# Optimization experiments

Hardware: AMD Instinct MI355X
Metric: run time of the kernel (lower is better)

The kernel has to match this reference:

```python
import jax, jax.numpy as jnp
import numpy as np

B, IN_DIM, T, H = 16384, 4096, 6, 256
ALPHA = 0.1


def _prune_l1(w, amount=0.5):
    # emulate torch.nn.utils.prune.l1_unstructured: zero the smallest-|w| fraction
    thr = jnp.quantile(jnp.abs(w).reshape(w.shape[0], -1), amount, axis=1)
    thr = thr.reshape((w.shape[0],) + (1,) * (w.ndim - 1))
    return jnp.where(jnp.abs(w) >= thr, w, 0.0)


def setup_inputs() -> dict:
    key = jax.random.key(0)
    ks = jax.random.split(key, 12)
    s1 = 1.0 / np.sqrt(IN_DIM)
    s2 = 1.0 / np.sqrt(H)
    headW1 = jax.random.uniform(ks[0], (T, H, IN_DIM), minval=-s1, maxval=s1)
    headW1 = _prune_l1(headW1, 0.5)  # prune applied to first Linear of each head
    headb1 = jax.random.uniform(ks[1], (T, H), minval=-s1, maxval=s1)
    headW2 = jax.random.uniform(ks[2], (T, H, H), minval=-s2, maxval=s2)
    headb2 = jax.random.uniform(ks[3], (T, H), minval=-s2, maxval=s2)
    task_queries = jax.random.normal(ks[4], (T, H))
    keyW = jax.random.uniform(ks[5], (H, H), minval=-s2, maxval=s2)
    keyb = jax.random.uniform(ks[6], (H,), minval=-s2, maxval=s2)
    valW = jax.random.uniform(ks[7], (H, H), minval=-s2, maxval=s2)
    valb = jax.random.uniform(ks[8], (H,), minval=-s2, maxval=s2)
    bias = jnp.asarray(2.0, dtype=jnp.float32)
    x = jax.random.normal(ks[9], (B, IN_DIM), dtype=jnp.float32)
    return {"x": x, "headW1": headW1, "headb1": headb1, "headW2": headW2,
            "headb2": headb2, "task_queries": task_queries, "keyW": keyW,
            "keyb": keyb, "valW": valW, "valb": valb, "bias": bias}


def reference(x, headW1, headb1, headW2, headb2, task_queries, keyW, keyb, valW, valb, bias):
    # per-task heads (all heads see the full feature set): [B,T,H]
    h = jax.nn.relu(jnp.einsum("bi,thi->bth", x, headW1) + headb1)
    h = jax.nn.relu(jnp.einsum("bth,toh->bto", h, headW2) + headb2)
    K = jnp.einsum("bth,oh->bto", h, keyW) + keyb  # [B,T,H]
    V = jnp.einsum("bth,oh->bto", h, valW) + valb  # [B,T,H]
    logits = jnp.einsum("qh,bkh->bqk", task_queries, K) / jnp.sqrt(jnp.float32(H))
    m = logits.max(axis=2, keepdims=True) + 1e-8
    W_s = jax.nn.softmax(jnp.eye(T, dtype=logits.dtype) + ALPHA * (logits / m), axis=2)
    attended = jnp.einsum("bqk,bkh->bqh", W_s, V)  # [B,T,H]
    y1_logits = attended.mean(axis=-1)  # [B,T]
    y1_probs = jax.nn.sigmoid(y1_logits - bias)
    return jnp.clip(y1_probs, 1e-7, 1.0 - 1e-7)
```

## Files before the change

### kernel.cpp

```cpp
#include <hip/hip_runtime.h>
#include <hip/hip_bf16.h>


typedef float    f32x4 __attribute__((ext_vector_type(4)));
typedef short    s16x8 __attribute__((ext_vector_type(8)));
typedef unsigned short u16x4 __attribute__((ext_vector_type(4)));

__global__ void M3H_64587718197825_kernel() {}

__device__ __forceinline__ unsigned short bf16rn(float x) {
    unsigned u = __float_as_uint(x);
    return (unsigned short)((u + 0x7FFFu + ((u >> 16) & 1u)) >> 16);
}
__device__ __forceinline__ float bf16tof(unsigned short h) {
    return __uint_as_float(((unsigned)h) << 16);
}


__device__ __forceinline__ void stage_lds16(const unsigned short* src, int ld,
                                            unsigned short* lds, int tid)
{
#pragma unroll
    for (int t = 0; t < 2; ++t) {
        int c  = t * 256 + tid;
        int r  = c >> 2;
        int cr = c & 3;
        int s  = (r + (r >> 2)) & 3;
        long long g = (long long)r * ld + ((cr ^ s) << 3);
        __builtin_amdgcn_global_load_lds(
            (const __attribute__((address_space(1))) unsigned int*)(const void*)(src + g),
            (__attribute__((address_space(3))) unsigned int*)(void*)(lds + (c << 3)),
            16, 0, 0);
    }
}

__device__ __forceinline__ void stage_split_a(const float* Atile, int lda,
                                              unsigned short* sAh, unsigned short* sAl,
                                              int tid)
{
    int r = tid >> 1;
    int h = tid & 1;
    const float* ap = Atile + (long long)r * lda + (h << 4);
    float4 v0 = *(const float4*)(ap + 0);
    float4 v1 = *(const float4*)(ap + 4);
    float4 v2 = *(const float4*)(ap + 8);
    float4 v3 = *(const float4*)(ap + 12);
    float xs[16];
    xs[0]=v0.x; xs[1]=v0.y; xs[2]=v0.z;  xs[3]=v0.w;
    xs[4]=v1.x; xs[5]=v1.y; xs[6]=v1.z;  xs[7]=v1.w;
    xs[8]=v2.x; xs[9]=v2.y; xs[10]=v2.z; xs[11]=v2.w;
    xs[12]=v3.x; xs[13]=v3.y; xs[14]=v3.z; xs[15]=v3.w;
    s16x8 hv0, hv1, lv0, lv1;
#pragma unroll
    for (int i = 0; i < 8; ++i) {
        unsigned short hb = bf16rn(xs[i]);
        hv0[i] = (short)hb;
        lv0[i] = (short)bf16rn(xs[i] - bf16tof(hb));
    }
#pragma unroll
    for (int i = 0; i < 8; ++i) {
        unsigned short hb = bf16rn(xs[8 + i]);
        hv1[i] = (short)hb;
        lv1[i] = (short)bf16rn(xs[8 + i] - bf16tof(hb));
    }
    int s  = (r + (r >> 2)) & 3;
    int c0 = ((h << 1) | 0) ^ s;
    int c1 = ((h << 1) | 1) ^ s;
    int base = r << 5;
    *(s16x8*)(sAh + base + (c0 << 3)) = hv0;
    *(s16x8*)(sAh + base + (c1 << 3)) = hv1;
    *(s16x8*)(sAl + base + (c0 << 3)) = lv0;
    *(s16x8*)(sAl + base + (c1 << 3)) = lv1;
}

template<bool SPLIT_A, bool WRITE_SPLIT>
__global__ __launch_bounds__(256, 4) void gemm_bf16x3(
    const float* A32, const unsigned short* Ah, const unsigned short* Al,
    const unsigned short* Bh, const unsigned short* Bl,
    const float* bias, float* C32, unsigned short* Ch, unsigned short* Cl,
    int K, int lda, int ldb, int ldc,
    long long aOffZ, long long bOffZ, long long cOffZ, long long biasOffZ)
{
    int z = blockIdx.z;
    if constexpr (SPLIT_A) {
        A32 += (long long)z * aOffZ;
    } else {
        Ah += (long long)z * aOffZ;
        Al += (long long)z * aOffZ;
    }
    Bh += (long long)z * bOffZ;
    Bl += (long long)z * bOffZ;
    bias += (long long)z * biasOffZ;
    if constexpr (WRITE_SPLIT) {
        Ch += (long long)z * cOffZ;
        Cl += (long long)z * cOffZ;
    } else {
        C32 += (long long)z * cOffZ;
    }

    __shared__ __attribute__((aligned(16))) unsigned short sAh[4096];
    __shared__ __attribute__((aligned(16))) unsigned short sAl[4096];
    __shared__ __attribute__((aligned(16))) unsigned short sBh[4096];
    __shared__ __attribute__((aligned(16))) unsigned short sBl[4096];

    int nwg = gridDim.x * gridDim.y;
    int lin = blockIdx.y * gridDim.x + blockIdx.x;
    int qq = nwg >> 3, rr = nwg & 7;
    int xcd = lin & 7, idx = lin >> 3;
    int swz = (xcd < rr ? xcd * (qq + 1) : rr * (qq + 1) + (xcd - rr) * qq) + idx;
    const int tm = (swz / gridDim.x) * 128;
    const int tn = (swz % gridDim.x) * 128;

    const int tid  = threadIdx.x;
    const int lane = tid & 63;
    const int wid  = tid >> 6;
    const int wm = (wid & 1) << 6;
    const int wn = (wid >> 1) << 6;
    const int fr = lane & 15;
    const int fk = lane >> 4;
    const int swz8 = ((fk ^ ((fr + (fr >> 2)) & 3)) << 3);

    f32x4 acc[4][4];
    const f32x4 zero = {0.f, 0.f, 0.f, 0.f};
#pragma unroll
    for (int i = 0; i < 4; ++i)
#pragma unroll
        for (int j = 0; j < 4; ++j)
            acc[i][j] = zero;

    for (int k0 = 0; k0 < K; k0 += 32) {
        if constexpr (SPLIT_A) {
            stage_split_a(A32 + (long long)tm * lda + k0, lda, sAh, sAl, tid);
        } else {
            stage_lds16(Ah + (long long)tm * lda + k0, lda, sAh, tid);
            stage_lds16(Al + (long long)tm * lda + k0, lda, sAl, tid);
        }
        stage_lds16(Bh + (long long)tn * ldb + k0, ldb, sBh, tid);
        stage_lds16(Bl + (long long)tn * ldb + k0, ldb, sBl, tid);
        __syncthreads();

        s16x8 bh[4], bl[4];
#pragma unroll
        for (int ni = 0; ni < 4; ++ni) {
            int off = (wn + ni * 16 + fr) * 32 + swz8;
            bh[ni] = *(const s16x8*)(sBh + off);
            bl[ni] = *(const s16x8*)(sBl + off);
        }
#pragma unroll
        for (int mi = 0; mi < 4; ++mi) {
            int off = (wm + mi * 16 + fr) * 32 + swz8;
            s16x8 ah = *(const s16x8*)(sAh + off);
            s16x8 al = *(const s16x8*)(sAl + off);
#pragma unroll
            for (int ni = 0; ni < 4; ++ni) {
                acc[mi][ni] = __builtin_amdgcn_mfma_f32_16x16x32_bf16(ah, bh[ni], acc[mi][ni], 0, 0, 0);
                acc[mi][ni] = __builtin_amdgcn_mfma_f32_16x16x32_bf16(ah, bl[ni], acc[mi][ni], 0, 0, 0);
                acc[mi][ni] = __builtin_amdgcn_mfma_f32_16x16x32_bf16(al, bh[ni], acc[mi][ni], 0, 0, 0);
            }
        }
        __syncthreads();
    }

#pragma unroll
    for (int mi = 0; mi < 4; ++mi) {
        int crow = tm + wm + mi * 16 + fk * 4;
#pragma unroll
        for (int ni = 0; ni < 4; ++ni) {
            int ccol = tn + wn + ni * 16 + fr;
            float bv = bias[ccol];
#pragma unroll
            for (int rr2 = 0; rr2 < 4; ++rr2) {
                float v = acc[mi][ni][rr2] + bv;
                v = v > 0.f ? v : 0.f;
                long long ci = (long long)(crow + rr2) * ldc + ccol;
                if constexpr (WRITE_SPLIT) {
                    unsigned short hb = bf16rn(v);
                    Ch[ci] = hb;
                    Cl[ci] = bf16rn(v - bf16tof(hb));
                } else {
                    C32[ci] = v;
                }
            }
        }
    }
}

__global__ void split_ws(const float* in, unsigned short* hi, unsigned short* lo, int n4)
{
    for (int i = blockIdx.x * 256 + threadIdx.x; i < n4; i += gridDim.x * 256) {
        float4 v = ((const float4*)in)[i];
        float xs[4] = {v.x, v.y, v.z, v.w};
        u16x4 hv, lv;
#pragma unroll
        for (int j = 0; j < 4; ++j) {
            unsigned short hb = bf16rn(xs[j]);
            hv[j] = hb;
            lv[j] = bf16rn(xs[j] - bf16tof(hb));
        }
        ((u16x4*)hi)[i] = hv;
        ((u16x4*)lo)[i] = lv;
    }
}

__global__ void precompute(const float* tq, const float* keyW, const float* keyb,
                           const float* valW, const float* valb,
                           float* qk, float* qb, float* vbar, float* vbbar)
{
    __shared__ float tqs[1536];
    int h = threadIdx.x;
    for (int i = h; i < 1536; i += 256) tqs[i] = tq[i];
    __syncthreads();
    float acc0 = 0.f, acc1 = 0.f, acc2 = 0.f, acc3 = 0.f, acc4 = 0.f, acc5 = 0.f;
    float vb = 0.f;
    for (int o = 0; o < 256; ++o) {
        float kw = keyW[o * 256 + h];
        float vw = valW[o * 256 + h];
        acc0 += tqs[0 * 256 + o] * kw;
        acc1 += tqs[1 * 256 + o] * kw;
        acc2 += tqs[2 * 256 + o] * kw;
        acc3 += tqs[3 * 256 + o] * kw;
        acc4 += tqs[4 * 256 + o] * kw;
        acc5 += tqs[5 * 256 + o] * kw;
        vb += vw;
    }
    qk[0 * 256 + h] = acc0;
    qk[1 * 256 + h] = acc1;
    qk[2 * 256 + h] = acc2;
    qk[3 * 256 + h] = acc3;
    qk[4 * 256 + h] = acc4;
    qk[5 * 256 + h] = acc5;
    vbar[h] = vb * (1.0f / 256.0f);
    if (h < 6) {
        float s = 0.f;
        for (int o = 0; o < 256; ++o) s += tq[h * 256 + o] * keyb[o];
        qb[h] = s;
    }
    if (h == 6) {
        float s = 0.f;
        for (int o = 0; o < 256; ++o) s += valb[o];
        vbbar[0] = s * (1.0f / 256.0f);
    }
}

__global__ void dots(const float* h2, const float* qk, const float* qb,
                     const float* vbar, const float* vbbar,
                     float* L, float* Vm)
{
    __shared__ float U[7][256];
    __shared__ float qbs[8];
    int tid = threadIdx.x;
    for (int i = tid; i < 1792; i += 256)
        U[i >> 8][i & 255] = (i < 1536) ? qk[i] : vbar[i & 255];
    if (tid < 6) qbs[tid] = qb[tid];
    if (tid == 6) qbs[6] = vbbar[0];
    __syncthreads();
    int row = blockIdx.x * 256 + tid;
    const float* hr = h2 + (long long)row * 256;
    float a0 = 0.f, a1 = 0.f, a2 = 0.f, a3 = 0.f, a4 = 0.f, a5 = 0.f, a6 = 0.f;
    for (int i = 0; i < 256; i += 4) {
        float4 v = *(const float4*)(hr + i);
        float xs[4];
        xs[0] = v.x; xs[1] = v.y; xs[2] = v.z; xs[3] = v.w;
        for (int j = 0; j < 4; ++j) {
            float x = xs[j];
            int c = i + j;
            a0 += x * U[0][c];
            a1 += x * U[1][c];
            a2 += x * U[2][c];
            a3 += x * U[3][c];
            a4 += x * U[4][c];
            a5 += x * U[5][c];
            a6 += x * U[6][c];
        }
    }
    int b = row / 6, k = row - b * 6;
    float* Lr = L + (long long)b * 36 + k;
    Lr[0 * 6]  = (a0 + qbs[0]) * 0.0625f;
    Lr[1 * 6]  = (a1 + qbs[1]) * 0.0625f;
    Lr[2 * 6]  = (a2 + qbs[2]) * 0.0625f;
    Lr[3 * 6]  = (a3 + qbs[3]) * 0.0625f;
    Lr[4 * 6]  = (a4 + qbs[4]) * 0.0625f;
    Lr[5 * 6]  = (a5 + qbs[5]) * 0.0625f;
    Vm[row] = a6 + qbs[6];
}

__global__ void attn(const float* L, const float* Vm, const float* biasp, float* out)
{
    int b = blockIdx.x * 256 + threadIdx.x;
    float bias = biasp[0];
    float l[36], vm[6];
    const float* Lr = L + (long long)b * 36;
    for (int i = 0; i < 36; ++i) l[i] = Lr[i];
    for (int k = 0; k < 6; ++k) vm[k] = Vm[(long long)b * 6 + k];
    for (int q = 0; q < 6; ++q) {
        float m = l[q * 6];
        for (int k = 1; k < 6; ++k) m = fmaxf(m, l[q * 6 + k]);
        m += 1e-8f;
        float arg[6];
        float mx = -3.402823e38f;
        for (int k = 0; k < 6; ++k) {
            arg[k] = (k == q ? 1.0f : 0.0f) + 0.1f * l[q * 6 + k] / m;
            mx = fmaxf(mx, arg[k]);
        }
        float s = 0.f, y = 0.f;
        for (int k = 0; k < 6; ++k) {
            float e = expf(arg[k] - mx);
            s += e;
            y += e * vm[k];
        }
        y /= s;
        float p = 1.0f / (1.0f + expf(-(y - bias)));
        p = fminf(fmaxf(p, 1e-7f), 1.0f - 1e-7f);
        out[(long long)b * 6 + q] = p;
    }
}

extern "C" void kernel_launch(void* const* d_in, const int* in_sizes, int n_in,
                              void* d_out, int out_size, void* d_ws, size_t ws_size,
                              hipStream_t stream)
{
    const float* x      = (const float*)d_in[0];
    const float* headW1 = (const float*)d_in[1];
    const float* headb1 = (const float*)d_in[2];
    const float* headW2 = (const float*)d_in[3];
    const float* headb2 = (const float*)d_in[4];
    const float* tq     = (const float*)d_in[5];
    const float* keyW   = (const float*)d_in[6];
    const float* keyb   = (const float*)d_in[7];
    const float* valW   = (const float*)d_in[8];
    const float* valb   = (const float*)d_in[9];
    const float* biasp  = (const float*)d_in[10];
    float* out = (float*)d_out;

    char* w = (char*)d_ws;
    float* qk    = (float*)(w + 0);
    float* vbar  = (float*)(w + 6144);
    float* qb    = (float*)(w + 7168);
    float* vbbar = (float*)(w + 7200);
    unsigned short* h1h = (unsigned short*)(w + 8192);
    unsigned short* h1l = (unsigned short*)(w + 50339840LL);
    float* h2 = (float*)(w + 100671488LL);
    float* L  = (float*)(w + 201334784LL);
    float* Vm = (float*)(w + 203694080LL);
    unsigned short* w1h = (unsigned short*)(w + 204087296LL);
    unsigned short* w1l = (unsigned short*)(w + 216670208LL);
    unsigned short* w2h = (unsigned short*)(w + 229253120LL);
    unsigned short* w2l = (unsigned short*)(w + 230039552LL);

    split_ws<<<1024, 256, 0, stream>>>(headW1, w1h, w1l, 1572864);
    split_ws<<<384,  256, 0, stream>>>(headW2, w2h, w2l, 98304);

    precompute<<<1, 256, 0, stream>>>(tq, keyW, keyb, valW, valb, qk, qb, vbar, vbbar);

    gemm_bf16x3<true, true><<<dim3(12, 128, 1), 256, 0, stream>>>(
        x, nullptr, nullptr, w1h, w1l, headb1, nullptr, h1h, h1l,
        4096, 4096, 4096, 1536, 0, 0, 0, 0);

    gemm_bf16x3<false, false><<<dim3(2, 128, 6), 256, 0, stream>>>(
        nullptr, h1h, h1l, w2h, w2l, headb2, h2, nullptr, nullptr,
        256, 1536, 256, 1536, 256, 65536, 256, 256);

    dots<<<384, 256, 0, stream>>>(h2, qk, qb, vbar, vbbar, L, Vm);
    attn<<<64, 256, 0, stream>>>(L, Vm, biasp, out);
}
```

Before: 1.113 ms.

## Double-buffer LDS tiles to overlap next-tile loads with MFMA compute

Converts the GEMM main loop to a two-stage ping-pong LDS pipeline. The next K-tile's global-to-LDS loads (and the fp32 A loads, held in registers and split into bf16 after compute) are issued before the MFMA work on the current tile, and one barrier per iteration is removed. The aim is to hide global memory latency behind compute. In exchange, LDS use doubles to 64KB and launch bounds drop to 2 blocks per CU, which lowers occupancy and raises register pressure.

```diff
diff --git a/kernel.cpp b/kernel.cpp
--- a/kernel.cpp
+++ b/kernel.cpp
@@ -34,22 +34,32 @@
     }
 }
 
-__device__ __forceinline__ void stage_split_a(const float* Atile, int lda,
-                                              unsigned short* sAh, unsigned short* sAl,
-                                              int tid)
+struct AReg { float4 v0, v1, v2, v3; };
+
+__device__ __forceinline__ AReg stage_a_load(const float* Atile, int lda, int tid)
 {
     int r = tid >> 1;
     int h = tid & 1;
     const float* ap = Atile + (long long)r * lda + (h << 4);
-    float4 v0 = *(const float4*)(ap + 0);
-    float4 v1 = *(const float4*)(ap + 4);
-    float4 v2 = *(const float4*)(ap + 8);
-    float4 v3 = *(const float4*)(ap + 12);
+    AReg a;
+    a.v0 = *(const float4*)(ap + 0);
+    a.v1 = *(const float4*)(ap + 4);
+    a.v2 = *(const float4*)(ap + 8);
+    a.v3 = *(const float4*)(ap + 12);
+    return a;
+}
+
+__device__ __forceinline__ void stage_a_write(const AReg& a,
+                                              unsigned short* sAh, unsigned short* sAl,
+                                              int tid)
+{
+    int r = tid >> 1;
+    int h = tid & 1;
     float xs[16];
-    xs[0]=v0.x; xs[1]=v0.y; xs[2]=v0.z;  xs[3]=v0.w;
-    xs[4]=v1.x; xs[5]=v1.y; xs[6]=v1.z;  xs[7]=v1.w;
-    xs[8]=v2.x; xs[9]=v2.y; xs[10]=v2.z; xs[11]=v2.w;
-    xs[12]=v3.x; xs[13]=v3.y; xs[14]=v3.z; xs[15]=v3.w;
+    xs[0]=a.v0.x; xs[1]=a.v0.y; xs[2]=a.v0.z;  xs[3]=a.v0.w;
+    xs[4]=a.v1.x; xs[5]=a.v1.y; xs[6]=a.v1.z;  xs[7]=a.v1.w;
+    xs[8]=a.v2.x; xs[9]=a.v2.y; xs[10]=a.v2.z; xs[11]=a.v2.w;
+    xs[12]=a.v3.x; xs[13]=a.v3.y; xs[14]=a.v3.z; xs[15]=a.v3.w;
     s16x8 hv0, hv1, lv0, lv1;
 #pragma unroll
     for (int i = 0; i < 8; ++i) {
@@ -74,7 +84,7 @@
 }
 
 template<bool SPLIT_A, bool WRITE_SPLIT>
-__global__ __launch_bounds__(256, 4) void gemm_bf16x3(
+__global__ __launch_bounds__(256, 2) void gemm_bf16x3(
     const float* A32, const unsigned short* Ah, const unsigned short* Al,
     const unsigned short* Bh, const unsigned short* Bl,
     const float* bias, float* C32, unsigned short* Ch, unsigned short* Cl,
@@ -98,10 +108,10 @@
         C32 += (long long)z * cOffZ;
     }
 
-    __shared__ __attribute__((aligned(16))) unsigned short sAh[4096];
-    __shared__ __attribute__((aligned(16))) unsigned short sAl[4096];
-    __shared__ __attribute__((aligned(16))) unsigned short sBh[4096];
-    __shared__ __attribute__((aligned(16))) unsigned short sBl[4096];
+    __shared__ __attribute__((aligned(16))) unsigned short sAh[2][4096];
+    __shared__ __attribute__((aligned(16))) unsigned short sAl[2][4096];
+    __shared__ __attribute__((aligned(16))) unsigned short sBh[2][4096];
+    __shared__ __attribute__((aligned(16))) unsigned short sBl[2][4096];
 
     int nwg = gridDim.x * gridDim.y;
     int lin = blockIdx.y * gridDim.x + blockIdx.x;
@@ -120,6 +130,12 @@
     const int fk = lane >> 4;
     const int swz8 = ((fk ^ ((fr + (fr >> 2)) & 3)) << 3);
 
+    const float* aBase = SPLIT_A ? (A32 + (long long)tm * lda) : nullptr;
+    const unsigned short* ahBase = SPLIT_A ? nullptr : (Ah + (long long)tm * lda);
+    const unsigned short* alBase = SPLIT_A ? nullptr : (Al + (long long)tm * lda);
+    const unsigned short* bhBase = Bh + (long long)tn * ldb;
+    const unsigned short* blBase = Bl + (long long)tn * ldb;
+
     f32x4 acc[4][4];
     const f32x4 zero = {0.f, 0.f, 0.f, 0.f};
 #pragma unroll
@@ -128,35 +144,57 @@
         for (int j = 0; j < 4; ++j)
             acc[i][j] = zero;
 
-    for (int k0 = 0; k0 < K; k0 += 32) {
-        if constexpr (SPLIT_A) {
-            stage_split_a(A32 + (long long)tm * lda + k0, lda, sAh, sAl, tid);
-        } else {
-            stage_lds16(Ah + (long long)tm * lda + k0, lda, sAh, tid);
-            stage_lds16(Al + (long long)tm * lda + k0, lda, sAl, tid);
-        }
-        stage_lds16(Bh + (long long)tn * ldb + k0, ldb, sBh, tid);
-        stage_lds16(Bl + (long long)tn * ldb + k0, ldb, sBl, tid);
-        __syncthreads();
+    if constexpr (SPLIT_A) {
+        AReg a0 = stage_a_load(aBase, lda, tid);
+        stage_a_write(a0, sAh[0], sAl[0], tid);
+    } else {
+        stage_lds16(ahBase, lda, sAh[0], tid);
+        stage_lds16(alBase, lda, sAl[0], tid);
+    }
+    stage_lds16(bhBase, ldb, sBh[0], tid);
+    stage_lds16(blBase, ldb, sBl[0], tid);
+    __syncthreads();
+
+    const int nt = K >> 5;
+    for (int t = 0; t < nt; ++t) {
+        const int P = t & 1, Q = P ^ 1;
+        const bool pf = (t + 1 < nt);
+        const int k1 = (t + 1) << 5;
+
+        AReg nxt;
+        if (pf) {
+            if constexpr (SPLIT_A) {
+                nxt = stage_a_load(aBase + k1, lda, tid);
+            } else {
+                stage_lds16(ahBase + k1, lda, sAh[Q], tid);
+                stage_lds16(alBase + k1, lda, sAl[Q], tid);
+            }
+            stage_lds16(bhBase + k1, ldb, sBh[Q], tid);
+            stage_lds16(blBase + k1, ldb, sBl[Q], tid);
+        }
 
         s16x8 bh[4], bl[4];
 #pragma unroll
         for (int ni = 0; ni < 4; ++ni) {
             int off = (wn + ni * 16 + fr) * 32 + swz8;
-            bh[ni] = *(const s16x8*)(sBh + off);
-            bl[ni] = *(const s16x8*)(sBl + off);
+            bh[ni] = *(const s16x8*)(sBh[P] + off);
+            bl[ni] = *(const s16x8*)(sBl[P] + off);
         }
 #pragma unroll
         for (int mi = 0; mi < 4; ++mi) {
             int off = (wm + mi * 16 + fr) * 32 + swz8;
-            s16x8 ah = *(const s16x8*)(sAh + off);
-            s16x8 al = *(const s16x8*)(sAl + off);
+            s16x8 ah = *(const s16x8*)(sAh[P] + off);
+            s16x8 al = *(const s16x8*)(sAl[P] + off);
 #pragma unroll
             for (int ni = 0; ni < 4; ++ni) {
                 acc[mi][ni] = __builtin_amdgcn_mfma_f32_16x16x32_bf16(ah, bh[ni], acc[mi][ni], 0, 0, 0);
                 acc[mi][ni] = __builtin_amdgcn_mfma_f32_16x16x32_bf16(ah, bl[ni], acc[mi][ni], 0, 0, 0);
                 acc[mi][ni] = __builtin_amdgcn_mfma_f32_16x16x32_bf16(al, bh[ni], acc[mi][ni], 0, 0, 0);
             }
+        }
+
+        if constexpr (SPLIT_A) {
+            if (pf) stage_a_write(nxt, sAh[Q], sAl[Q], tid);
         }
         __syncthreads();
     }
```

Result: slower. 1.219 ms (+9.6%).

## Fuse key/value projection dots into second GEMM epilogue with atomic accumulation

Applied to the files above, without the earlier changes.

The second GEMM's epilogue now applies bias and ReLU, projects each output row onto the six query-key vectors and the mean value vector, reduces across lanes with shuffles, and atomically adds into L and Vm. This removes the fp32 h2 round trip through memory and the separate dots kernel. A zeroing kernel for L/Vm is added, precompute is spread over 7 blocks, and launch bounds drop from 4 to 2 waves per SIMD, which may lower occupancy in the first GEMM. Atomic float adds make the summation order nondeterministic.

```diff
diff --git a/kernel.cpp b/kernel.cpp
--- a/kernel.cpp
+++ b/kernel.cpp
@@ -73,11 +73,13 @@
     *(s16x8*)(sAl + base + (c1 << 3)) = lv1;
 }
 
-template<bool SPLIT_A, bool WRITE_SPLIT>
-__global__ __launch_bounds__(256, 4) void gemm_bf16x3(
+template<bool SPLIT_A, bool WRITE_SPLIT, bool FUSE>
+__global__ __launch_bounds__(256, 2) void gemm_bf16x3(
     const float* A32, const unsigned short* Ah, const unsigned short* Al,
     const unsigned short* Bh, const unsigned short* Bl,
     const float* bias, float* C32, unsigned short* Ch, unsigned short* Cl,
+    const float* qk, const float* qb, const float* vbar, const float* vbbar,
+    float* L, float* Vm,
     int K, int lda, int ldb, int ldc,
     long long aOffZ, long long bOffZ, long long cOffZ, long long biasOffZ)
 {
@@ -94,7 +96,7 @@
     if constexpr (WRITE_SPLIT) {
         Ch += (long long)z * cOffZ;
         Cl += (long long)z * cOffZ;
-    } else {
+    } else if constexpr (!FUSE) {
         C32 += (long long)z * cOffZ;
     }
 
@@ -161,24 +163,72 @@
         __syncthreads();
     }
 
-#pragma unroll
-    for (int mi = 0; mi < 4; ++mi) {
-        int crow = tm + wm + mi * 16 + fk * 4;
+    if constexpr (FUSE) {
+        float Ur[4][7];
+        float biasv[4];
 #pragma unroll
         for (int ni = 0; ni < 4; ++ni) {
             int ccol = tn + wn + ni * 16 + fr;
-            float bv = bias[ccol];
-#pragma unroll
-            for (int rr2 = 0; rr2 < 4; ++rr2) {
-                float v = acc[mi][ni][rr2] + bv;
+            biasv[ni] = bias[ccol];
+#pragma unroll
+            for (int j = 0; j < 6; ++j) Ur[ni][j] = qk[j * 256 + ccol];
+            Ur[ni][6] = vbar[ccol];
+        }
+        float qbl = 0.f;
+        if (fr < 6) qbl = qb[fr];
+        else if (fr == 6) qbl = vbbar[0];
+        const bool addc = ((tn + wn) == 0);
+#pragma unroll
+        for (int r = 0; r < 16; ++r) {
+            const int mi = r >> 2, rr2 = r & 3;
+            int brow = tm + wm + mi * 16 + fk * 4 + rr2;
+            float p[7] = {0.f, 0.f, 0.f, 0.f, 0.f, 0.f, 0.f};
+#pragma unroll
+            for (int ni = 0; ni < 4; ++ni) {
+                float v = acc[mi][ni][rr2] + biasv[ni];
                 v = v > 0.f ? v : 0.f;
-                long long ci = (long long)(crow + rr2) * ldc + ccol;
-                if constexpr (WRITE_SPLIT) {
-                    unsigned short hb = bf16rn(v);
-                    Ch[ci] = hb;
-                    Cl[ci] = bf16rn(v - bf16tof(hb));
-                } else {
-                    C32[ci] = v;
+#pragma unroll
+                for (int j = 0; j < 7; ++j) p[j] += v * Ur[ni][j];
+            }
+#pragma unroll
+            for (int m = 1; m < 16; m <<= 1)
+#pragma unroll
+                for (int j = 0; j < 7; ++j) p[j] += __shfl_xor(p[j], m, 64);
+            float mine = p[0];
+            mine = (fr == 1) ? p[1] : mine;
+            mine = (fr == 2) ? p[2] : mine;
+            mine = (fr == 3) ? p[3] : mine;
+            mine = (fr == 4) ? p[4] : mine;
+            mine = (fr == 5) ? p[5] : mine;
+            mine = (fr == 6) ? p[6] : mine;
+            if (fr < 6) {
+                float val = (mine + (addc ? qbl : 0.f)) * 0.0625f;
+                atomicAdd(&L[(long long)brow * 36 + fr * 6 + z], val);
+            } else if (fr == 6) {
+                float val = mine + (addc ? qbl : 0.f);
+                atomicAdd(&Vm[(long long)brow * 6 + z], val);
+            }
+        }
+    } else {
+#pragma unroll
+        for (int mi = 0; mi < 4; ++mi) {
+            int crow = tm + wm + mi * 16 + fk * 4;
+#pragma unroll
+            for (int ni = 0; ni < 4; ++ni) {
+                int ccol = tn + wn + ni * 16 + fr;
+                float bv = bias[ccol];
+#pragma unroll
+                for (int rr2 = 0; rr2 < 4; ++rr2) {
+                    float v = acc[mi][ni][rr2] + bv;
+                    v = v > 0.f ? v : 0.f;
+                    long long ci = (long long)(crow + rr2) * ldc + ccol;
+                    if constexpr (WRITE_SPLIT) {
+                        unsigned short hb = bf16rn(v);
+                        Ch[ci] = hb;
+                        Cl[ci] = bf16rn(v - bf16tof(hb));
+                    } else {
+                        C32[ci] = v;
+                    }
                 }
             }
         }
@@ -202,86 +252,46 @@
     }
 }
 
+__global__ void zeroLV(float4* p)
+{
+    p[blockIdx.x * 256 + threadIdx.x] = float4{0.f, 0.f, 0.f, 0.f};
+}
+
 __global__ void precompute(const float* tq, const float* keyW, const float* keyb,
                            const float* valW, const float* valb,
                            float* qk, float* qb, float* vbar, float* vbbar)
 {
-    __shared__ float tqs[1536];
+    __shared__ float tqs[256];
+    __shared__ float red[256];
     int h = threadIdx.x;
-    for (int i = h; i < 1536; i += 256) tqs[i] = tq[i];
-    __syncthreads();
-    float acc0 = 0.f, acc1 = 0.f, acc2 = 0.f, acc3 = 0.f, acc4 = 0.f, acc5 = 0.f;
-    float vb = 0.f;
-    for (int o = 0; o < 256; ++o) {
-        float kw = keyW[o * 256 + h];
-        float vw = valW[o * 256 + h];
-        acc0 += tqs[0 * 256 + o] * kw;
-        acc1 += tqs[1 * 256 + o] * kw;
-        acc2 += tqs[2 * 256 + o] * kw;
-        acc3 += tqs[3 * 256 + o] * kw;
-        acc4 += tqs[4 * 256 + o] * kw;
-        acc5 += tqs[5 * 256 + o] * kw;
-        vb += vw;
-    }
-    qk[0 * 256 + h] = acc0;
-    qk[1 * 256 + h] = acc1;
-    qk[2 * 256 + h] = acc2;
-    qk[3 * 256 + h] = acc3;
-    qk[4 * 256 + h] = acc4;
-    qk[5 * 256 + h] = acc5;
-    vbar[h] = vb * (1.0f / 256.0f);
-    if (h < 6) {
-        float s = 0.f;
-        for (int o = 0; o < 256; ++o) s += tq[h * 256 + o] * keyb[o];
-        qb[h] = s;
-    }
-    if (h == 6) {
-        float s = 0.f;
-        for (int o = 0; o < 256; ++o) s += valb[o];
-        vbbar[0] = s * (1.0f / 256.0f);
-    }
-}
-
-__global__ void dots(const float* h2, const float* qk, const float* qb,
-                     const float* vbar, const float* vbbar,
-                     float* L, float* Vm)
-{
-    __shared__ float U[7][256];
-    __shared__ float qbs[8];
-    int tid = threadIdx.x;
-    for (int i = tid; i < 1792; i += 256)
-        U[i >> 8][i & 255] = (i < 1536) ? qk[i] : vbar[i & 255];
-    if (tid < 6) qbs[tid] = qb[tid];
-    if (tid == 6) qbs[6] = vbbar[0];
-    __syncthreads();
-    int row = blockIdx.x * 256 + tid;
-    const float* hr = h2 + (long long)row * 256;
-    float a0 = 0.f, a1 = 0.f, a2 = 0.f, a3 = 0.f, a4 = 0.f, a5 = 0.f, a6 = 0.f;
-    for (int i = 0; i < 256; i += 4) {
-        float4 v = *(const float4*)(hr + i);
-        float xs[4];
-        xs[0] = v.x; xs[1] = v.y; xs[2] = v.z; xs[3] = v.w;
-        for (int j = 0; j < 4; ++j) {
-            float x = xs[j];
-            int c = i + j;
-            a0 += x * U[0][c];
-            a1 += x * U[1][c];
-            a2 += x * U[2][c];
-            a3 += x * U[3][c];
-            a4 += x * U[4][c];
-            a5 += x * U[5][c];
-            a6 += x * U[6][c];
-        }
-    }
-    int b = row / 6, k = row - b * 6;
-    float* Lr = L + (long long)b * 36 + k;
-    Lr[0 * 6]  = (a0 + qbs[0]) * 0.0625f;
-    Lr[1 * 6]  = (a1 + qbs[1]) * 0.0625f;
-    Lr[2 * 6]  = (a2 + qbs[2]) * 0.0625f;
-    Lr[3 * 6]  = (a3 + qbs[3]) * 0.0625f;
-    Lr[4 * 6]  = (a4 + qbs[4]) * 0.0625f;
-    Lr[5 * 6]  = (a5 + qbs[5]) * 0.0625f;
-    Vm[row] = a6 + qbs[6];
+    int blk = blockIdx.x;
+    if (blk < 6) {
+        tqs[h] = tq[blk * 256 + h];
+        __syncthreads();
+        float acc = 0.f;
+        for (int o = 0; o < 256; ++o)
+            acc += tqs[o] * keyW[o * 256 + h];
+        qk[blk * 256 + h] = acc;
+        red[h] = tqs[h] * keyb[h];
+        __syncthreads();
+        for (int s = 128; s > 0; s >>= 1) {
+            if (h < s) red[h] += red[h + s];
+            __syncthreads();
+        }
+        if (h == 0) qb[blk] = red[0];
+    } else {
+        float vb = 0.f;
+        for (int o = 0; o < 256; ++o)
+            vb += valW[o * 256 + h];
+        vbar[h] = vb * (1.0f / 256.0f);
+        red[h] = valb[h];
+        __syncthreads();
+        for (int s = 128; s > 0; s >>= 1) {
+            if (h < s) red[h] += red[h + s];
+            __syncthreads();
+        }
+        if (h == 0) vbbar[0] = red[0] * (1.0f / 256.0f);
+    }
 }
 
 __global__ void attn(const float* L, const float* Vm, const float* biasp, float* out)
@@ -339,7 +349,6 @@
     float* vbbar = (float*)(w + 7200);
     unsigned short* h1h = (unsigned short*)(w + 8192);
     unsigned short* h1l = (unsigned short*)(w + 50339840LL);
-    float* h2 = (float*)(w + 100671488LL);
     float* L  = (float*)(w + 201334784LL);
     float* Vm = (float*)(w + 203694080LL);
     unsigned short* w1h = (unsigned short*)(w + 204087296LL);
@@ -350,16 +359,19 @@
     split_ws<<<1024, 256, 0, stream>>>(headW1, w1h, w1l, 1572864);
     split_ws<<<384,  256, 0, stream>>>(headW2, w2h, w2l, 98304);
 
-    precompute<<<1, 256, 0, stream>>>(tq, keyW, keyb, valW, valb, qk, qb, vbar, vbbar);
-
-    gemm_bf16x3<true, true><<<dim3(12, 128, 1), 256, 0, stream>>>(
+    precompute<<<7, 256, 0, stream>>>(tq, keyW, keyb, valW, valb, qk, qb, vbar, vbbar);
+
+    zeroLV<<<672, 256, 0, stream>>>((float4*)L);
+
+    gemm_bf16x3<true, true, false><<<dim3(12, 128, 1), 256, 0, stream>>>(
         x, nullptr, nullptr, w1h, w1l, headb1, nullptr, h1h, h1l,
+        nullptr, nullptr, nullptr, nullptr, nullptr, nullptr,
         4096, 4096, 4096, 1536, 0, 0, 0, 0);
 
-    gemm_bf16x3<false, false><<<dim3(2, 128, 6), 256, 0, stream>>>(
-        nullptr, h1h, h1l, w2h, w2l, headb2, h2, nullptr, nullptr,
-        256, 1536, 256, 1536, 256, 65536, 256, 256);
-
-    dots<<<384, 256, 0, stream>>>(h2, qk, qb, vbar, vbbar, L, Vm);
+    gemm_bf16x3<false, false, true><<<dim3(2, 128, 6), 256, 0, stream>>>(
+        nullptr, h1h, h1l, w2h, w2l, headb2, nullptr, nullptr, nullptr,
+        qk, qb, vbar, vbbar, L, Vm,
+        256, 1536, 256, 0, 256, 65536, 0, 256);
+
     attn<<<64, 256, 0, stream>>>(L, Vm, biasp, out);
 }
```

Result: faster. 1.024 ms (-7.9%).
